# Performance work log

Hardware: AMD Instinct MI355X
Metric: run time of the kernel (lower is better)

## Reference

```python
import jax, jax.numpy as jnp
import numpy as np

N = 50000      # total nodes (25 graphs x 2000 proteins)
E = 1200000    # total edges
G = 25         # graphs
F_IN = 128     # protein_features
H = 64         # hidden_dim
L = 2          # num_layers


def setup_inputs() -> dict:
    key = jax.random.key(0)
    ks = jax.random.split(key, 24)
    inp = {
        "x": jax.random.normal(ks[0], (N, F_IN), dtype=jnp.float32),
        "edge_attr": jax.random.uniform(ks[1], (E,), dtype=jnp.float32),
        "global_features": jax.random.normal(ks[2], (G, 6), dtype=jnp.float32),
        "edge_index": jax.random.randint(ks[3], (2, E), 0, N, dtype=jnp.int64),
        "batch": (jnp.arange(N, dtype=jnp.int64) // (N // G)),
    }
    s = 0.05
    inp["W_embed"] = jax.random.normal(ks[4], (F_IN, H), dtype=jnp.float32) * s
    inp["b_embed"] = jnp.zeros((H,), dtype=jnp.float32)
    inp["W_glob"] = jax.random.normal(ks[5], (6, H), dtype=jnp.float32) * s
    inp["b_glob"] = jnp.zeros((H,), dtype=jnp.float32)
    # stacked per-layer GATConv params (heads=1)
    inp["lin_W"] = jax.random.normal(ks[6], (L, H, H), dtype=jnp.float32) * s
    inp["att_src"] = jax.random.normal(ks[7], (L, H), dtype=jnp.float32) * s
    inp["att_dst"] = jax.random.normal(ks[8], (L, H), dtype=jnp.float32) * s
    inp["lin_edge_W"] = jax.random.normal(ks[9], (L, 1, H), dtype=jnp.float32) * s
    inp["att_edge"] = jax.random.normal(ks[10], (L, H), dtype=jnp.float32) * s
    inp["gat_bias"] = jnp.zeros((L, H), dtype=jnp.float32)
    inp["W_comb"] = jax.random.normal(ks[11], (2 * H, H), dtype=jnp.float32) * s
    inp["b_comb"] = jnp.zeros((H,), dtype=jnp.float32)
    inp["W_out"] = jax.random.normal(ks[12], (H, 1), dtype=jnp.float32) * s
    inp["b_out"] = jnp.zeros((1,), dtype=jnp.float32)
    return inp


def _forward(x, edge_attr, global_features, W_embed, b_embed, W_glob, b_glob,
             lin_W, att_src, att_dst, lin_edge_W, att_edge, gat_bias,
             W_comb, b_comb, W_out, b_out, edge_index, batch):
    src, dst = edge_index[0], edge_index[1]
    h = x @ W_embed + b_embed                       # [N,H]
    g = global_features @ W_glob + b_glob           # [G,H]
    ea = edge_attr[:, None]                         # [E,1] (edge_attr.unsqueeze(1))
    for l in range(L):
        hs = h @ lin_W[l]                           # [N,H] shared lin_src/lin_dst
        a_src = hs @ att_src[l]                     # [N]
        a_dst = hs @ att_dst[l]                     # [N]
        ef = ea @ lin_edge_W[l]                     # [E,H]
        a_edge = ef @ att_edge[l]                   # [E]
        alpha = jax.nn.leaky_relu(a_src[src] + a_dst[dst] + a_edge, 0.2)
        # segment softmax over incoming edges of each dst node
        m = jax.ops.segment_max(alpha, dst, num_segments=N)
        ex = jnp.exp(alpha - m[dst])
        denom = jax.ops.segment_sum(ex, dst, num_segments=N)
        alpha = ex / (denom[dst] + 1e-16)
        msg = alpha[:, None] * hs[src]              # [E,H]
        h = jax.ops.segment_sum(msg, dst, num_segments=N) + gat_bias[l]
        h = jax.nn.relu(h)
    # global_mean_pool
    counts = jax.ops.segment_sum(jnp.ones((N,), h.dtype), batch, num_segments=G)
    graph = jax.ops.segment_sum(h, batch, num_segments=G) / counts[:, None]
    combined = jax.nn.relu(jnp.concatenate([graph, g], axis=1) @ W_comb + b_comb)
    return combined @ W_out + b_out                 # [G,1]


def reference(x, edge_attr, global_features, W_embed, b_embed, W_glob, b_glob,
              lin_W, att_src, att_dst, lin_edge_W, att_edge, gat_bias,
              W_comb, b_comb, W_out, b_out, edge_index, batch):
    return _forward(x, edge_attr, global_features, W_embed, b_embed, W_glob, b_glob,
                    lin_W, att_src, att_dst, lin_edge_W, att_edge, gat_bias,
                    W_comb, b_comb, W_out, b_out, edge_index, batch)
```

## Files before the change

kernel.cpp:

```cpp
#include <hip/hip_runtime.h>
#include <hip/hip_fp16.h>
#include <math.h>

#define N_NODES 50000
#define N_EDGES 1200000
#define N_GRAPH 25
#define F_IN 128
#define H_DIM 64
#define NODES_PER_GRAPH 2000
#define POOL_CHUNKS 32

#define NBUCK 196
#define BUCK_CAP 8000
#define EPB 4096
#define NB_BIN ((N_EDGES + EPB - 1) / EPB)
#define NB_GEMM ((N_NODES + 63) / 64)

#define OFF_H     0
#define OFF_HS    (N_NODES*64)
#define OFF_ASRC  (OFF_HS + N_NODES*64)
#define OFF_ADST  (OFF_ASRC + N_NODES)
#define OFF_CBUF  (OFF_ADST + N_NODES)
#define OFF_BCUR  (OFF_CBUF + 16)
#define OFF_GSUM  (OFF_BCUR + 256)
#define OFF_ROWP  (OFF_GSUM + N_GRAPH*64)
#define OFF_ESRT  (OFF_ROWP + N_NODES + 2)
#define OFF_EL2   (OFF_ESRT + N_EDGES)
#define OFF_STAGE (OFF_EL2 + 2*N_EDGES)

__global__ __launch_bounds__(256) void k_embed(const float* __restrict__ x,
                                               const float* __restrict__ W,
                                               const float* __restrict__ b,
                                               float* __restrict__ h,
                                               const float* __restrict__ linE,
                                               const float* __restrict__ attE,
                                               float* __restrict__ cbuf,
                                               int* __restrict__ bcur,
                                               float* __restrict__ gsum) {
    __shared__ float4 sW4[F_IN * 16];
    __shared__ float4 sx4[64 * 17];
    int tid = threadIdx.x;
    if (blockIdx.x == 0) {
        for (int i = tid; i < 256; i += 256) bcur[i] = 0;
        for (int i = tid; i < N_GRAPH * 64; i += 256) gsum[i] = 0.f;
        if (tid < 128) {
            int l = tid >> 6, j = tid & 63;
            float v = linE[l * 64 + j] * attE[l * 64 + j];
            #pragma unroll
            for (int m = 1; m < 64; m <<= 1) v += __shfl_xor(v, m);
            if (j == 0) cbuf[l] = v;
        }
    }
    int n0 = blockIdx.x * 64;
    const float4* W4 = (const float4*)W;
    const float4* x4 = (const float4*)x;
    #pragma unroll
    for (int i = 0; i < 8; ++i) sW4[tid + i * 256] = W4[tid + i * 256];

    int c4 = tid & 15, ng = tid >> 4;
    int r = tid >> 4, q = tid & 15;
    float4 acc[4];
    #pragma unroll
    for (int j = 0; j < 4; ++j) acc[j] = make_float4(0.f, 0.f, 0.f, 0.f);

    for (int kh = 0; kh < 2; ++kh) {
        __syncthreads();
        #pragma unroll
        for (int rb = 0; rb < 4; ++rb) {
            int rr = r + rb * 16;
            int n = n0 + rr;
            float4 v = make_float4(0.f, 0.f, 0.f, 0.f);
            if (n < N_NODES) v = x4[(size_t)n * 32 + kh * 16 + q];
            sx4[rr * 17 + q] = v;
        }
        __syncthreads();
        #pragma unroll
        for (int kq = 0; kq < 16; ++kq) {
            float4 wv[4];
            #pragma unroll
            for (int kk = 0; kk < 4; ++kk) wv[kk] = sW4[(kh * 64 + kq * 4 + kk) * 16 + c4];
            #pragma unroll
            for (int j = 0; j < 4; ++j) {
                float4 xv = sx4[(ng * 4 + j) * 17 + kq];
                float xs[4] = {xv.x, xv.y, xv.z, xv.w};
                #pragma unroll
                for (int kk = 0; kk < 4; ++kk) {
                    acc[j].x = fmaf(xs[kk], wv[kk].x, acc[j].x);
                    acc[j].y = fmaf(xs[kk], wv[kk].y, acc[j].y);
                    acc[j].z = fmaf(xs[kk], wv[kk].z, acc[j].z);
                    acc[j].w = fmaf(xs[kk], wv[kk].w, acc[j].w);
                }
            }
        }
    }
    float4 bb = ((const float4*)b)[c4];
    #pragma unroll
    for (int j = 0; j < 4; ++j) {
        int n = n0 + ng * 4 + j;
        if (n < N_NODES) {
            float4 v;
            v.x = acc[j].x + bb.x; v.y = acc[j].y + bb.y;
            v.z = acc[j].z + bb.z; v.w = acc[j].w + bb.w;
            ((float4*)h)[(size_t)n * 16 + c4] = v;
        }
    }
}

__global__ __launch_bounds__(256) void k_hs(const float* __restrict__ hin,
                                            const float* __restrict__ W,
                                            const float* __restrict__ attS,
                                            const float* __restrict__ attD,
                                            __half* __restrict__ hs_h,
                                            float* __restrict__ asrc,
                                            float* __restrict__ adst) {
    __shared__ float4 sW4[H_DIM * 16];
    __shared__ float4 sx4[64 * 17];
    int tid = threadIdx.x;
    int n0 = blockIdx.x * 64;
    const float4* W4 = (const float4*)W;
    const float4* h4 = (const float4*)hin;
    #pragma unroll
    for (int i = 0; i < 4; ++i) sW4[tid + i * 256] = W4[tid + i * 256];
    int r = tid >> 4, q = tid & 15;
    #pragma unroll
    for (int rb = 0; rb < 4; ++rb) {
        int rr = r + rb * 16;
        int n = n0 + rr;
        float4 v = make_float4(0.f, 0.f, 0.f, 0.f);
        if (n < N_NODES) v = h4[(size_t)n * 16 + q];
        sx4[rr * 17 + q] = v;
    }
    __syncthreads();

    int c4 = tid & 15, ng = tid >> 4;
    float4 acc[4];
    #pragma unroll
    for (int j = 0; j < 4; ++j) acc[j] = make_float4(0.f, 0.f, 0.f, 0.f);
    #pragma unroll
    for (int kq = 0; kq < 16; ++kq) {
        float4 wv[4];
        #pragma unroll
        for (int kk = 0; kk < 4; ++kk) wv[kk] = sW4[(kq * 4 + kk) * 16 + c4];
        #pragma unroll
        for (int j = 0; j < 4; ++j) {
            float4 xv = sx4[(ng * 4 + j) * 17 + kq];
            float xs[4] = {xv.x, xv.y, xv.z, xv.w};
            #pragma unroll
            for (int kk = 0; kk < 4; ++kk) {
                acc[j].x = fmaf(xs[kk], wv[kk].x, acc[j].x);
                acc[j].y = fmaf(xs[kk], wv[kk].y, acc[j].y);
                acc[j].z = fmaf(xs[kk], wv[kk].z, acc[j].z);
                acc[j].w = fmaf(xs[kk], wv[kk].w, acc[j].w);
            }
        }
    }
    float4 aS = ((const float4*)attS)[c4];
    float4 aD = ((const float4*)attD)[c4];
    #pragma unroll
    for (int j = 0; j < 4; ++j) {
        int n = n0 + ng * 4 + j;
        float rs = acc[j].x * aS.x + acc[j].y * aS.y + acc[j].z * aS.z + acc[j].w * aS.w;
        float rd = acc[j].x * aD.x + acc[j].y * aD.y + acc[j].z * aD.z + acc[j].w * aD.w;
        #pragma unroll
        for (int o = 1; o < 16; o <<= 1) {
            rs += __shfl_xor(rs, o);
            rd += __shfl_xor(rd, o);
        }
        if (n < N_NODES) {
            __half2 p0 = __floats2half2_rn(acc[j].x, acc[j].y);
            __half2 p1 = __floats2half2_rn(acc[j].z, acc[j].w);
            uint2 st;
            st.x = *(unsigned*)&p0;
            st.y = *(unsigned*)&p1;
            ((uint2*)hs_h)[(size_t)n * 16 + c4] = st;
            if (c4 == 0) { asrc[n] = rs; adst[n] = rd; }
        }
    }
}

__global__ __launch_bounds__(256) void k_el(const unsigned* __restrict__ esrt,
                                            const float* __restrict__ asrc,
                                            const float* __restrict__ cbuf,
                                            int layer,
                                            uint2* __restrict__ el2) {
    int e = blockIdx.x * 256 + threadIdx.x;
    if (e >= N_EDGES) return;
    unsigned v = esrt[e];
    unsigned s = v & 0xFFFFu;
    float eav = __uint_as_float(v & 0xFFFF0000u);
    float lg = asrc[s] + cbuf[layer] * eav;
    uint2 r; r.x = __float_as_uint(lg); r.y = s;
    el2[e] = r;
}

__device__ __forceinline__ int block_excl_scan(int v, int tid, int* lds, int* total) {
    int lane = tid & 63, w = tid >> 6;
    int incl = v;
    #pragma unroll
    for (int off = 1; off < 64; off <<= 1) {
        int t = __shfl_up(incl, off);
        if (lane >= off) incl += t;
    }
    if (lane == 63) lds[w] = incl;
    __syncthreads();
    int wo = 0;
    for (int i = 0; i < w; ++i) wo += lds[i];
    *total = lds[0] + lds[1] + lds[2] + lds[3];
    __syncthreads();
    return wo + incl - v;
}

__global__ __launch_bounds__(256) void k_bin(const int* __restrict__ ei,
                                             const float* __restrict__ ea,
                                             uint2* __restrict__ stage,
                                             int* __restrict__ bcur) {
    __shared__ int lcnt[NBUCK];
    __shared__ int lbase[NBUCK];
    int tid = threadIdx.x;
    for (int i = tid; i < NBUCK; i += 256) lcnt[i] = 0;
    __syncthreads();
    int e0 = blockIdx.x * EPB;
    unsigned pw0[16], pw1[16];
    #pragma unroll
    for (int k = 0; k < 16; ++k) {
        int e = e0 + k * 256 + tid;
        bool ok = e < N_EDGES;
        int s = ok ? ei[e] : 0;
        int d = ok ? ei[N_EDGES + e] : 0;
        float v = ok ? ea[e] : 0.f;
        pw0[k] = (unsigned)s | ((unsigned)d << 16);
        pw1[k] = __float_as_uint(v);
        if (ok) atomicAdd(&lcnt[d >> 8], 1);
    }
    __syncthreads();
    for (int i = tid; i < NBUCK; i += 256) {
        lbase[i] = atomicAdd(&bcur[i], lcnt[i]);
        lcnt[i] = 0;
    }
    __syncthreads();
    #pragma unroll
    for (int k = 0; k < 16; ++k) {
        int e = e0 + k * 256 + tid;
        if (e < N_EDGES) {
            int b = pw0[k] >> 24;
            int pos = lbase[b] + atomicAdd(&lcnt[b], 1);
            uint2 t; t.x = pw0[k]; t.y = pw1[k];
            stage[b * BUCK_CAP + pos] = t;
        }
    }
}

__global__ __launch_bounds__(256) void k_group(const uint2* __restrict__ stage,
                                               const int* __restrict__ bcur,
                                               int* __restrict__ rowp,
                                               unsigned* __restrict__ esrt,
                                               const float* __restrict__ asrc,
                                               const float* __restrict__ cbuf,
                                               uint2* __restrict__ el2) {
    int b = blockIdx.x;
    int tid = threadIdx.x;
    __shared__ int sprefix[256];
    __shared__ int lcnt[256];
    __shared__ int lofs[256];
    __shared__ int slds[4];
    int bv = (tid < NBUCK) ? bcur[tid] : 0;
    int total;
    int bex = block_excl_scan(bv, tid, slds, &total);
    sprefix[tid] = bex;
    lcnt[tid] = 0;
    __syncthreads();
    int base = sprefix[b];
    int cntb = bcur[b];
    float c0 = cbuf[0];
    const uint2* reg = stage + b * BUCK_CAP;
    for (int i = tid; i < cntb; i += 256)
        atomicAdd(&lcnt[(reg[i].x >> 16) & 255], 1);
    __syncthreads();
    int ex = block_excl_scan(lcnt[tid], tid, slds, &total);
    lofs[tid] = base + ex;
    int n = b * 256 + tid;
    if (n < N_NODES) rowp[n] = base + ex;
    if (b == 0 && tid == 0) rowp[N_NODES] = N_EDGES;
    __syncthreads();
    lcnt[tid] = 0;
    __syncthreads();
    for (int i = tid; i < cntb; i += 256) {
        uint2 v = reg[i];
        int dloc = (v.x >> 16) & 255;
        int pos = lofs[dloc] + atomicAdd(&lcnt[dloc], 1);
        unsigned s = v.x & 0xFFFFu;
        unsigned eab = (v.y + 0x8000u) & 0xFFFF0000u;
        esrt[pos] = s | eab;
        float lg = asrc[s] + c0 * __uint_as_float(eab);
        uint2 r; r.x = __float_as_uint(lg); r.y = s;
        el2[pos] = r;
    }
}

__global__ __launch_bounds__(256) void k_fused(const int* __restrict__ rowp,
                                               const uint2* __restrict__ el2,
                                               const float* __restrict__ adst,
                                               const __half* __restrict__ hs_h,
                                               int layer,
                                               const float* __restrict__ gbias,
                                               float* __restrict__ hout) {
    int pair = (blockIdx.x * 256 + threadIdx.x) >> 6;
    int lane = threadIdx.x & 63;
    int half = lane >> 5, l32 = lane & 31;
    int wid = pair * 2 + half;
    if (wid >= N_NODES) return;
    int beg = rowp[wid], end = rowp[wid + 1];
    float adv = adst[wid];
    float psum = 0.f;
    float acc[8];
    #pragma unroll
    for (int j = 0; j < 8; ++j) acc[j] = 0.f;
    int g = (lane >> 3) & 3;
    int fl8 = lane & 7;
    int hb = half * 32;
    const uint4* hsq = (const uint4*)hs_h;

#define UNPACK_FMA(w_, r_)                                                      \
    {                                                                           \
        __half2 h0_ = *(__half2*)&r_.x, h1_ = *(__half2*)&r_.y;                 \
        __half2 h2_ = *(__half2*)&r_.z, h3_ = *(__half2*)&r_.w;                 \
        float2 f0_ = __half22float2(h0_), f1_ = __half22float2(h1_);            \
        float2 f2_ = __half22float2(h2_), f3_ = __half22float2(h3_);            \
        acc[0] = fmaf(w_, f0_.x, acc[0]); acc[1] = fmaf(w_, f0_.y, acc[1]);     \
        acc[2] = fmaf(w_, f1_.x, acc[2]); acc[3] = fmaf(w_, f1_.y, acc[3]);     \
        acc[4] = fmaf(w_, f2_.x, acc[4]); acc[5] = fmaf(w_, f2_.y, acc[5]);     \
        acc[6] = fmaf(w_, f3_.x, acc[6]); acc[7] = fmaf(w_, f3_.y, acc[7]);     \
    }

    for (int base = beg; base < end; base += 32) {
        int idx = base + l32;
        bool ok = idx < end;
        float exv = 0.f;
        int s = 0;
        if (ok) {
            uint2 v = el2[idx];
            s = (int)v.y;
            float a = __uint_as_float(v.x) + adv;
            a = a >= 0.f ? a : 0.2f * a;
            exv = __expf(a);
        }
        psum += exv;

        int lim = end - base; if (lim > 32) lim = 32;
        int t = g;
        for (; t + 12 < lim; t += 16) {
            float w0 = __shfl(exv, hb + t),      w1 = __shfl(exv, hb + t + 4);
            float w2 = __shfl(exv, hb + t + 8),  w3 = __shfl(exv, hb + t + 12);
            int   s0 = __shfl(s, hb + t),        s1 = __shfl(s, hb + t + 4);
            int   s2 = __shfl(s, hb + t + 8),    s3 = __shfl(s, hb + t + 12);
            uint4 r0 = hsq[s0 * 8 + fl8];
            uint4 r1 = hsq[s1 * 8 + fl8];
            uint4 r2 = hsq[s2 * 8 + fl8];
            uint4 r3 = hsq[s3 * 8 + fl8];
            UNPACK_FMA(w0, r0);
            UNPACK_FMA(w1, r1);
            UNPACK_FMA(w2, r2);
            UNPACK_FMA(w3, r3);
        }
        for (; t < lim; t += 4) {
            float w0 = __shfl(exv, hb + t);
            int   s0 = __shfl(s, hb + t);
            uint4 r0 = hsq[s0 * 8 + fl8];
            UNPACK_FMA(w0, r0);
        }
    }
#undef UNPACK_FMA
    #pragma unroll
    for (int o = 1; o < 32; o <<= 1) psum += __shfl_xor(psum, o);
    #pragma unroll
    for (int o = 8; o < 32; o <<= 1) {
        #pragma unroll
        for (int j = 0; j < 8; ++j) acc[j] += __shfl_xor(acc[j], o);
    }

    if (l32 < 8) {
        float inv = 1.f / (psum + 1e-16f);
        const float* gb = gbias + layer * H_DIM + l32 * 8;
        float* op = hout + (size_t)wid * H_DIM + l32 * 8;
        float4 v0, v1;
        v0.x = acc[0] * inv + gb[0]; v0.x = v0.x > 0.f ? v0.x : 0.f;
        v0.y = acc[1] * inv + gb[1]; v0.y = v0.y > 0.f ? v0.y : 0.f;
        v0.z = acc[2] * inv + gb[2]; v0.z = v0.z > 0.f ? v0.z : 0.f;
        v0.w = acc[3] * inv + gb[3]; v0.w = v0.w > 0.f ? v0.w : 0.f;
        v1.x = acc[4] * inv + gb[4]; v1.x = v1.x > 0.f ? v1.x : 0.f;
        v1.y = acc[5] * inv + gb[5]; v1.y = v1.y > 0.f ? v1.y : 0.f;
        v1.z = acc[6] * inv + gb[6]; v1.z = v1.z > 0.f ? v1.z : 0.f;
        v1.w = acc[7] * inv + gb[7]; v1.w = v1.w > 0.f ? v1.w : 0.f;
        ((float4*)op)[0] = v0;
        ((float4*)op)[1] = v1;
    }
}

__global__ __launch_bounds__(256) void k_pool(const float* __restrict__ h,
                                              float* __restrict__ gsum) {
    int g = blockIdx.x / POOL_CHUNKS;
    int chunk = blockIdx.x % POOL_CHUNKS;
    int wave = threadIdx.x >> 6, lane = threadIdx.x & 63;
    const int per_chunk = (NODES_PER_GRAPH + POOL_CHUNKS - 1) / POOL_CHUNKS;
    int n0 = g * NODES_PER_GRAPH + chunk * per_chunk;
    int n1 = g * NODES_PER_GRAPH + min((chunk + 1) * per_chunk, NODES_PER_GRAPH);
    float sum = 0.f;
    for (int n = n0 + wave; n < n1; n += 4)
        sum += h[(size_t)n * H_DIM + lane];
    __shared__ float spart[4][64];
    spart[wave][lane] = sum;
    __syncthreads();
    if (wave == 0) {
        float tot = spart[0][lane] + spart[1][lane] + spart[2][lane] + spart[3][lane];
        atomicAdd(gsum + g * H_DIM + lane, tot);
    }
}

__global__ __launch_bounds__(64) void k_head2(const float* __restrict__ gsum,
                                              const float* __restrict__ gf,
                                              const float* __restrict__ Wg,
                                              const float* __restrict__ bg,
                                              const float* __restrict__ Wc,
                                              const float* __restrict__ bc,
                                              const float* __restrict__ Wo,
                                              const float* __restrict__ bo,
                                              float* __restrict__ out) {
    int g = blockIdx.x;
    int lane = threadIdx.x;
    __shared__ float sgraph[64];
    __shared__ float sgf[64];
    sgraph[lane] = gsum[g * H_DIM + lane] / (float)NODES_PER_GRAPH;
    float gv = bg[lane];
    #pragma unroll
    for (int k = 0; k < 6; ++k) gv += gf[g * 6 + k] * Wg[k * 64 + lane];
    sgf[lane] = gv;
    __syncthreads();
    float cj = bc[lane];
    #pragma unroll
    for (int k = 0; k < 64; ++k) cj += sgraph[k] * Wc[k * 64 + lane];
    #pragma unroll
    for (int k = 0; k < 64; ++k) cj += sgf[k] * Wc[(64 + k) * 64 + lane];
    cj = cj > 0.f ? cj : 0.f;
    float o = cj * Wo[lane];
    #pragma unroll
    for (int m = 1; m < 64; m <<= 1) o += __shfl_xor(o, m);
    if (lane == 0) out[g] = o + bo[0];
}

extern "C" void kernel_launch(void* const* d_in, const int* in_sizes, int n_in,
                              void* d_out, int out_size, void* d_ws, size_t ws_size,
                              hipStream_t stream) {
    const float* x        = (const float*)d_in[0];
    const float* ea       = (const float*)d_in[1];
    const float* gf       = (const float*)d_in[2];
    const int*   ei       = (const int*)d_in[3];
    const float* W_embed  = (const float*)d_in[5];
    const float* b_embed  = (const float*)d_in[6];
    const float* W_glob   = (const float*)d_in[7];
    const float* b_glob   = (const float*)d_in[8];
    const float* lin_W    = (const float*)d_in[9];
    const float* att_src  = (const float*)d_in[10];
    const float* att_dst  = (const float*)d_in[11];
    const float* lin_eW   = (const float*)d_in[12];
    const float* att_edge = (const float*)d_in[13];
    const float* gat_bias = (const float*)d_in[14];
    const float* W_comb   = (const float*)d_in[15];
    const float* b_comb   = (const float*)d_in[16];
    const float* W_out    = (const float*)d_in[17];
    const float* b_out    = (const float*)d_in[18];
    float* out = (float*)d_out;
    float* ws  = (float*)d_ws;

    float*    h      = ws + OFF_H;
    __half*   hs_h   = (__half*)(ws + OFF_HS);
    float*    asrc   = ws + OFF_ASRC;
    float*    adst   = ws + OFF_ADST;
    float*    cbuf   = ws + OFF_CBUF;
    int*      bcur   = (int*)(ws + OFF_BCUR);
    float*    gsum   = ws + OFF_GSUM;
    int*      rowp   = (int*)(ws + OFF_ROWP);
    unsigned* esrt   = (unsigned*)(ws + OFF_ESRT);
    uint2*    el2    = (uint2*)(ws + OFF_EL2);
    uint2*    stage  = (uint2*)(ws + OFF_STAGE);

    const int egrid = (N_EDGES + 255) / 256;
    const int fgrid = (N_NODES / 2 + 3) / 4;

    k_embed<<<NB_GEMM, 256, 0, stream>>>(x, W_embed, b_embed, h,
                                         lin_eW, att_edge, cbuf, bcur, gsum);
    k_hs<<<NB_GEMM, 256, 0, stream>>>(h, lin_W,
                                      att_src, att_dst, hs_h, asrc, adst);

    k_bin<<<NB_BIN, 256, 0, stream>>>(ei, ea, stage, bcur);
    k_group<<<NBUCK, 256, 0, stream>>>(stage, bcur, rowp, esrt, asrc, cbuf, el2);

    k_fused<<<fgrid, 256, 0, stream>>>(rowp, el2, adst, hs_h, 0, gat_bias, h);
    k_hs<<<NB_GEMM, 256, 0, stream>>>(h, lin_W + 64 * 64,
                                      att_src + 64, att_dst + 64, hs_h, asrc, adst);
    k_el<<<egrid, 256, 0, stream>>>(esrt, asrc, cbuf, 1, el2);
    k_fused<<<fgrid, 256, 0, stream>>>(rowp, el2, adst, hs_h, 1, gat_bias, h);

    k_pool<<<N_GRAPH * POOL_CHUNKS, 256, 0, stream>>>(h, gsum);
    k_head2<<<N_GRAPH, 64, 0, stream>>>(gsum, gf, W_glob, b_glob,
                                        W_comb, b_comb, W_out, b_out, out);
}
```

Before: 187.6 us.

## Fuse embedding with first GAT projection and fold mean-pool into last aggregation

Merges the input embedding GEMM with the layer-0 linear projection and attention-logit computation in a single kernel, so the intermediate embedding is never written to or read back from global memory. The last-layer aggregation kernel now accumulates its ReLU outputs into a per-block shared sum and atomically adds it to the per-graph pool buffer, which removes the separate pooling kernel and the final h write/read. This trades extra shared memory in the embed kernel and shared and global atomics in the fused kernel for fewer launches and less global traffic. The grid for the aggregation kernel is now exactly N/8 blocks, so each block's 8 nodes map to a single graph.

```diff
diff --git a/kernel.cpp b/kernel.cpp
--- a/kernel.cpp
+++ b/kernel.cpp
@@ -8,7 +8,6 @@
 #define F_IN 128
 #define H_DIM 64
 #define NODES_PER_GRAPH 2000
-#define POOL_CHUNKS 32
 
 #define NBUCK 196
 #define BUCK_CAP 8000
@@ -28,16 +27,22 @@
 #define OFF_EL2   (OFF_ESRT + N_EDGES)
 #define OFF_STAGE (OFF_EL2 + 2*N_EDGES)
 
-__global__ __launch_bounds__(256) void k_embed(const float* __restrict__ x,
-                                               const float* __restrict__ W,
-                                               const float* __restrict__ b,
-                                               float* __restrict__ h,
-                                               const float* __restrict__ linE,
-                                               const float* __restrict__ attE,
-                                               float* __restrict__ cbuf,
-                                               int* __restrict__ bcur,
-                                               float* __restrict__ gsum) {
-    __shared__ float4 sW4[F_IN * 16];
+__global__ __launch_bounds__(256) void k_embed_hs(const float* __restrict__ x,
+                                                  const float* __restrict__ We,
+                                                  const float* __restrict__ be,
+                                                  const float* __restrict__ Wh,
+                                                  const float* __restrict__ attS,
+                                                  const float* __restrict__ attD,
+                                                  __half* __restrict__ hs_h,
+                                                  float* __restrict__ asrc,
+                                                  float* __restrict__ adst,
+                                                  const float* __restrict__ linE,
+                                                  const float* __restrict__ attE,
+                                                  float* __restrict__ cbuf,
+                                                  int* __restrict__ bcur,
+                                                  float* __restrict__ gsum) {
+    __shared__ float4 sWe[F_IN * 16];
+    __shared__ float4 sWh[H_DIM * 16];
     __shared__ float4 sx4[64 * 17];
     int tid = threadIdx.x;
     if (blockIdx.x == 0) {
@@ -52,10 +57,13 @@
         }
     }
     int n0 = blockIdx.x * 64;
-    const float4* W4 = (const float4*)W;
-    const float4* x4 = (const float4*)x;
-    #pragma unroll
-    for (int i = 0; i < 8; ++i) sW4[tid + i * 256] = W4[tid + i * 256];
+    const float4* We4 = (const float4*)We;
+    const float4* Wh4 = (const float4*)Wh;
+    const float4* x4  = (const float4*)x;
+    #pragma unroll
+    for (int i = 0; i < 8; ++i) sWe[tid + i * 256] = We4[tid + i * 256];
+    #pragma unroll
+    for (int i = 0; i < 4; ++i) sWh[tid + i * 256] = Wh4[tid + i * 256];
 
     int c4 = tid & 15, ng = tid >> 4;
     int r = tid >> 4, q = tid & 15;
@@ -78,7 +86,7 @@
         for (int kq = 0; kq < 16; ++kq) {
             float4 wv[4];
             #pragma unroll
-            for (int kk = 0; kk < 4; ++kk) wv[kk] = sW4[(kh * 64 + kq * 4 + kk) * 16 + c4];
+            for (int kk = 0; kk < 4; ++kk) wv[kk] = sWe[(kh * 64 + kq * 4 + kk) * 16 + c4];
             #pragma unroll
             for (int j = 0; j < 4; ++j) {
                 float4 xv = sx4[(ng * 4 + j) * 17 + kq];
@@ -93,15 +101,55 @@
             }
         }
     }
-    float4 bb = ((const float4*)b)[c4];
+    float4 bb = ((const float4*)be)[c4];
+    __syncthreads();
+    #pragma unroll
+    for (int j = 0; j < 4; ++j) {
+        float4 v;
+        v.x = acc[j].x + bb.x; v.y = acc[j].y + bb.y;
+        v.z = acc[j].z + bb.z; v.w = acc[j].w + bb.w;
+        sx4[(ng * 4 + j) * 17 + c4] = v;
+        acc[j] = make_float4(0.f, 0.f, 0.f, 0.f);
+    }
+    __syncthreads();
+    #pragma unroll
+    for (int kq = 0; kq < 16; ++kq) {
+        float4 wv[4];
+        #pragma unroll
+        for (int kk = 0; kk < 4; ++kk) wv[kk] = sWh[(kq * 4 + kk) * 16 + c4];
+        #pragma unroll
+        for (int j = 0; j < 4; ++j) {
+            float4 xv = sx4[(ng * 4 + j) * 17 + kq];
+            float xs[4] = {xv.x, xv.y, xv.z, xv.w};
+            #pragma unroll
+            for (int kk = 0; kk < 4; ++kk) {
+                acc[j].x = fmaf(xs[kk], wv[kk].x, acc[j].x);
+                acc[j].y = fmaf(xs[kk], wv[kk].y, acc[j].y);
+                acc[j].z = fmaf(xs[kk], wv[kk].z, acc[j].z);
+                acc[j].w = fmaf(xs[kk], wv[kk].w, acc[j].w);
+            }
+        }
+    }
+    float4 aS = ((const float4*)attS)[c4];
+    float4 aD = ((const float4*)attD)[c4];
     #pragma unroll
     for (int j = 0; j < 4; ++j) {
         int n = n0 + ng * 4 + j;
+        float rs = acc[j].x * aS.x + acc[j].y * aS.y + acc[j].z * aS.z + acc[j].w * aS.w;
+        float rd = acc[j].x * aD.x + acc[j].y * aD.y + acc[j].z * aD.z + acc[j].w * aD.w;
+        #pragma unroll
+        for (int o = 1; o < 16; o <<= 1) {
+            rs += __shfl_xor(rs, o);
+            rd += __shfl_xor(rd, o);
+        }
         if (n < N_NODES) {
-            float4 v;
-            v.x = acc[j].x + bb.x; v.y = acc[j].y + bb.y;
-            v.z = acc[j].z + bb.z; v.w = acc[j].w + bb.w;
-            ((float4*)h)[(size_t)n * 16 + c4] = v;
+            __half2 p0 = __floats2half2_rn(acc[j].x, acc[j].y);
+            __half2 p1 = __floats2half2_rn(acc[j].z, acc[j].w);
+            uint2 st;
+            st.x = *(unsigned*)&p0;
+            st.y = *(unsigned*)&p1;
+            ((uint2*)hs_h)[(size_t)n * 16 + c4] = st;
+            if (c4 == 0) { asrc[n] = rs; adst[n] = rd; }
         }
     }
 }
@@ -297,122 +345,121 @@
     }
 }
 
+template <bool POOL>
 __global__ __launch_bounds__(256) void k_fused(const int* __restrict__ rowp,
                                                const uint2* __restrict__ el2,
                                                const float* __restrict__ adst,
                                                const __half* __restrict__ hs_h,
                                                int layer,
                                                const float* __restrict__ gbias,
-                                               float* __restrict__ hout) {
-    int pair = (blockIdx.x * 256 + threadIdx.x) >> 6;
-    int lane = threadIdx.x & 63;
+                                               float* __restrict__ hout,
+                                               float* __restrict__ gsum) {
+    __shared__ float sblock[64];
+    int tid = threadIdx.x;
+    if (POOL) {
+        if (tid < 64) sblock[tid] = 0.f;
+        __syncthreads();
+    }
+    int pair = (blockIdx.x * 256 + tid) >> 6;
+    int lane = tid & 63;
     int half = lane >> 5, l32 = lane & 31;
     int wid = pair * 2 + half;
-    if (wid >= N_NODES) return;
-    int beg = rowp[wid], end = rowp[wid + 1];
-    float adv = adst[wid];
-    float psum = 0.f;
-    float acc[8];
-    #pragma unroll
-    for (int j = 0; j < 8; ++j) acc[j] = 0.f;
-    int g = (lane >> 3) & 3;
-    int fl8 = lane & 7;
-    int hb = half * 32;
-    const uint4* hsq = (const uint4*)hs_h;
+    if (wid < N_NODES) {
+        int beg = rowp[wid], end = rowp[wid + 1];
+        float adv = adst[wid];
+        float psum = 0.f;
+        float acc[8];
+        #pragma unroll
+        for (int j = 0; j < 8; ++j) acc[j] = 0.f;
+        int g = (lane >> 3) & 3;
+        int fl8 = lane & 7;
+        int hb = half * 32;
+        const uint4* hsq = (const uint4*)hs_h;
 
 #define UNPACK_FMA(w_, r_)                                                      \
-    {                                                                           \
-        __half2 h0_ = *(__half2*)&r_.x, h1_ = *(__half2*)&r_.y;                 \
-        __half2 h2_ = *(__half2*)&r_.z, h3_ = *(__half2*)&r_.w;                 \
-        float2 f0_ = __half22float2(h0_), f1_ = __half22float2(h1_);            \
-        float2 f2_ = __half22float2(h2_), f3_ = __half22float2(h3_);            \
-        acc[0] = fmaf(w_, f0_.x, acc[0]); acc[1] = fmaf(w_, f0_.y, acc[1]);     \
-        acc[2] = fmaf(w_, f1_.x, acc[2]); acc[3] = fmaf(w_, f1_.y, acc[3]);     \
-        acc[4] = fmaf(w_, f2_.x, acc[4]); acc[5] = fmaf(w_, f2_.y, acc[5]);     \
-        acc[6] = fmaf(w_, f3_.x, acc[6]); acc[7] = fmaf(w_, f3_.y, acc[7]);     \
-    }
-
-    for (int base = beg; base < end; base += 32) {
-        int idx = base + l32;
-        bool ok = idx < end;
-        float exv = 0.f;
-        int s = 0;
-        if (ok) {
-            uint2 v = el2[idx];
-            s = (int)v.y;
-            float a = __uint_as_float(v.x) + adv;
-            a = a >= 0.f ? a : 0.2f * a;
-            exv = __expf(a);
-        }
-        psum += exv;
-
-        int lim = end - base; if (lim > 32) lim = 32;
-        int t = g;
-        for (; t + 12 < lim; t += 16) {
-            float w0 = __shfl(exv, hb + t),      w1 = __shfl(exv, hb + t + 4);
-            float w2 = __shfl(exv, hb + t + 8),  w3 = __shfl(exv, hb + t + 12);
-            int   s0 = __shfl(s, hb + t),        s1 = __shfl(s, hb + t + 4);
-            int   s2 = __shfl(s, hb + t + 8),    s3 = __shfl(s, hb + t + 12);
-            uint4 r0 = hsq[s0 * 8 + fl8];
-            uint4 r1 = hsq[s1 * 8 + fl8];
-            uint4 r2 = hsq[s2 * 8 + fl8];
-            uint4 r3 = hsq[s3 * 8 + fl8];
-            UNPACK_FMA(w0, r0);
-            UNPACK_FMA(w1, r1);
-            UNPACK_FMA(w2, r2);
-            UNPACK_FMA(w3, r3);
-        }
-        for (; t < lim; t += 4) {
-            float w0 = __shfl(exv, hb + t);
-            int   s0 = __shfl(s, hb + t);
-            uint4 r0 = hsq[s0 * 8 + fl8];
-            UNPACK_FMA(w0, r0);
-        }
-    }
+        {                                                                       \
+            __half2 h0_ = *(__half2*)&r_.x, h1_ = *(__half2*)&r_.y;             \
+            __half2 h2_ = *(__half2*)&r_.z, h3_ = *(__half2*)&r_.w;             \
+            float2 f0_ = __half22float2(h0_), f1_ = __half22float2(h1_);        \
+            float2 f2_ = __half22float2(h2_), f3_ = __half22float2(h3_);        \
+            acc[0] = fmaf(w_, f0_.x, acc[0]); acc[1] = fmaf(w_, f0_.y, acc[1]); \
+            acc[2] = fmaf(w_, f1_.x, acc[2]); acc[3] = fmaf(w_, f1_.y, acc[3]); \
+            acc[4] = fmaf(w_, f2_.x, acc[4]); acc[5] = fmaf(w_, f2_.y, acc[5]); \
+            acc[6] = fmaf(w_, f3_.x, acc[6]); acc[7] = fmaf(w_, f3_.y, acc[7]); \
+        }
+
+        for (int base = beg; base < end; base += 32) {
+            int idx = base + l32;
+            bool ok = idx < end;
+            float exv = 0.f;
+            int s = 0;
+            if (ok) {
+                uint2 v = el2[idx];
+                s = (int)v.y;
+                float a = __uint_as_float(v.x) + adv;
+                a = a >= 0.f ? a : 0.2f * a;
+                exv = __expf(a);
+            }
+            psum += exv;
+
+            int lim = end - base; if (lim > 32) lim = 32;
+            int t = g;
+            for (; t + 12 < lim; t += 16) {
+                float w0 = __shfl(exv, hb + t),      w1 = __shfl(exv, hb + t + 4);
+                float w2 = __shfl(exv, hb + t + 8),  w3 = __shfl(exv, hb + t + 12);
+                int   s0 = __shfl(s, hb + t),        s1 = __shfl(s, hb + t + 4);
+                int   s2 = __shfl(s, hb + t + 8),    s3 = __shfl(s, hb + t + 12);
+                uint4 r0 = hsq[s0 * 8 + fl8];
+                uint4 r1 = hsq[s1 * 8 + fl8];
+                uint4 r2 = hsq[s2 * 8 + fl8];
+                uint4 r3 = hsq[s3 * 8 + fl8];
+                UNPACK_FMA(w0, r0);
+                UNPACK_FMA(w1, r1);
+                UNPACK_FMA(w2, r2);
+                UNPACK_FMA(w3, r3);
+            }
+            for (; t < lim; t += 4) {
+                float w0 = __shfl(exv, hb + t);
+                int   s0 = __shfl(s, hb + t);
+                uint4 r0 = hsq[s0 * 8 + fl8];
+                UNPACK_FMA(w0, r0);
+            }
+        }
 #undef UNPACK_FMA
-    #pragma unroll
-    for (int o = 1; o < 32; o <<= 1) psum += __shfl_xor(psum, o);
-    #pragma unroll
-    for (int o = 8; o < 32; o <<= 1) {
-        #pragma unroll
-        for (int j = 0; j < 8; ++j) acc[j] += __shfl_xor(acc[j], o);
-    }
-
-    if (l32 < 8) {
-        float inv = 1.f / (psum + 1e-16f);
-        const float* gb = gbias + layer * H_DIM + l32 * 8;
-        float* op = hout + (size_t)wid * H_DIM + l32 * 8;
-        float4 v0, v1;
-        v0.x = acc[0] * inv + gb[0]; v0.x = v0.x > 0.f ? v0.x : 0.f;
-        v0.y = acc[1] * inv + gb[1]; v0.y = v0.y > 0.f ? v0.y : 0.f;
-        v0.z = acc[2] * inv + gb[2]; v0.z = v0.z > 0.f ? v0.z : 0.f;
-        v0.w = acc[3] * inv + gb[3]; v0.w = v0.w > 0.f ? v0.w : 0.f;
-        v1.x = acc[4] * inv + gb[4]; v1.x = v1.x > 0.f ? v1.x : 0.f;
-        v1.y = acc[5] * inv + gb[5]; v1.y = v1.y > 0.f ? v1.y : 0.f;
-        v1.z = acc[6] * inv + gb[6]; v1.z = v1.z > 0.f ? v1.z : 0.f;
-        v1.w = acc[7] * inv + gb[7]; v1.w = v1.w > 0.f ? v1.w : 0.f;
-        ((float4*)op)[0] = v0;
-        ((float4*)op)[1] = v1;
-    }
-}
-
-__global__ __launch_bounds__(256) void k_pool(const float* __restrict__ h,
-                                              float* __restrict__ gsum) {
-    int g = blockIdx.x / POOL_CHUNKS;
-    int chunk = blockIdx.x % POOL_CHUNKS;
-    int wave = threadIdx.x >> 6, lane = threadIdx.x & 63;
-    const int per_chunk = (NODES_PER_GRAPH + POOL_CHUNKS - 1) / POOL_CHUNKS;
-    int n0 = g * NODES_PER_GRAPH + chunk * per_chunk;
-    int n1 = g * NODES_PER_GRAPH + min((chunk + 1) * per_chunk, NODES_PER_GRAPH);
-    float sum = 0.f;
-    for (int n = n0 + wave; n < n1; n += 4)
-        sum += h[(size_t)n * H_DIM + lane];
-    __shared__ float spart[4][64];
-    spart[wave][lane] = sum;
-    __syncthreads();
-    if (wave == 0) {
-        float tot = spart[0][lane] + spart[1][lane] + spart[2][lane] + spart[3][lane];
-        atomicAdd(gsum + g * H_DIM + lane, tot);
+        #pragma unroll
+        for (int o = 1; o < 32; o <<= 1) psum += __shfl_xor(psum, o);
+        #pragma unroll
+        for (int o = 8; o < 32; o <<= 1) {
+            #pragma unroll
+            for (int j = 0; j < 8; ++j) acc[j] += __shfl_xor(acc[j], o);
+        }
+
+        if (l32 < 8) {
+            float inv = 1.f / (psum + 1e-16f);
+            const float* gb = gbias + layer * H_DIM + l32 * 8;
+            float vals[8];
+            #pragma unroll
+            for (int j = 0; j < 8; ++j) {
+                float v = acc[j] * inv + gb[j];
+                vals[j] = v > 0.f ? v : 0.f;
+            }
+            if (POOL) {
+                #pragma unroll
+                for (int j = 0; j < 8; ++j)
+                    atomicAdd(&sblock[l32 * 8 + j], vals[j]);
+            } else {
+                float* op = hout + (size_t)wid * H_DIM + l32 * 8;
+                float4 v0 = make_float4(vals[0], vals[1], vals[2], vals[3]);
+                float4 v1 = make_float4(vals[4], vals[5], vals[6], vals[7]);
+                ((float4*)op)[0] = v0;
+                ((float4*)op)[1] = v1;
+            }
+        }
+    }
+    if (POOL) {
+        __syncthreads();
+        int gg = (blockIdx.x * 8) / NODES_PER_GRAPH;
+        if (tid < 64) atomicAdd(gsum + gg * H_DIM + tid, sblock[tid]);
     }
 }
 
@@ -484,23 +531,23 @@
     uint2*    stage  = (uint2*)(ws + OFF_STAGE);
 
     const int egrid = (N_EDGES + 255) / 256;
-    const int fgrid = (N_NODES / 2 + 3) / 4;
-
-    k_embed<<<NB_GEMM, 256, 0, stream>>>(x, W_embed, b_embed, h,
-                                         lin_eW, att_edge, cbuf, bcur, gsum);
-    k_hs<<<NB_GEMM, 256, 0, stream>>>(h, lin_W,
-                                      att_src, att_dst, hs_h, asrc, adst);
+    const int fgrid = N_NODES / 8;
+
+    k_embed_hs<<<NB_GEMM, 256, 0, stream>>>(x, W_embed, b_embed, lin_W,
+                                            att_src, att_dst, hs_h, asrc, adst,
+                                            lin_eW, att_edge, cbuf, bcur, gsum);
 
     k_bin<<<NB_BIN, 256, 0, stream>>>(ei, ea, stage, bcur);
     k_group<<<NBUCK, 256, 0, stream>>>(stage, bcur, rowp, esrt, asrc, cbuf, el2);
 
-    k_fused<<<fgrid, 256, 0, stream>>>(rowp, el2, adst, hs_h, 0, gat_bias, h);
+    k_fused<false><<<fgrid, 256, 0, stream>>>(rowp, el2, adst, hs_h, 0,
+                                              gat_bias, h, gsum);
     k_hs<<<NB_GEMM, 256, 0, stream>>>(h, lin_W + 64 * 64,
                                       att_src + 64, att_dst + 64, hs_h, asrc, adst);
     k_el<<<egrid, 256, 0, stream>>>(esrt, asrc, cbuf, 1, el2);
-    k_fused<<<fgrid, 256, 0, stream>>>(rowp, el2, adst, hs_h, 1, gat_bias, h);
-
-    k_pool<<<N_GRAPH * POOL_CHUNKS, 256, 0, stream>>>(h, gsum);
+    k_fused<true><<<fgrid, 256, 0, stream>>>(rowp, el2, adst, hs_h, 1,
+                                             gat_bias, h, gsum);
+
     k_head2<<<N_GRAPH, 64, 0, stream>>>(gsum, gf, W_glob, b_glob,
                                         W_comb, b_comb, W_out, b_out, out);
 }
```

Measured after the change: 204.1 us. +8.8%, slower.
